# Kernel optimization log

Measured on AMD Instinct MI355X. Metric: run time of the kernel, lower is better.

## Reference

```python
import jax, jax.numpy as jnp
import numpy as np

H = 16          # num_attention_heads
D = 64          # attention_head_size
BUCKET = 128    # bucket_size
MAX_BUCKETS = 32
TEMP = 0.75
SINKHORN_ITERS = 5
NOISE_KEY = 42  # fixed key for gumbel routing noise (deterministic reference)


def _sinkhorn_route(pl, W, key):
    # pl: [b,h,buckets,d] bucket summaries, W: [h,d,buckets]
    R = jnp.einsum('bhid,hdf->bhif', pl, W)  # [b,h,buckets,buckets]
    u = jax.random.uniform(key, R.shape, R.dtype)
    gumbel = -jnp.log(-jnp.log(u + 1e-6) + 1e-6)
    R = (R + gumbel) / TEMP
    for _ in range(SINKHORN_ITERS):
        R = R - jax.scipy.special.logsumexp(R, axis=-1, keepdims=True)
        R = R - jax.scipy.special.logsumexp(R, axis=-2, keepdims=True)
    return jnp.exp(R)


def setup_inputs() -> dict:
    key = jax.random.key(0)
    kq, kk, kv, kwk, kwv = jax.random.split(key, 5)
    q = jax.random.normal(kq, (64, 4096, 64), jnp.float32)
    k = jax.random.normal(kk, (64, 4096, 64), jnp.float32)
    v = jax.random.normal(kv, (64, 4096, 64), jnp.float32)
    W_keys = jax.random.normal(kwk, (H, D, MAX_BUCKETS), jnp.float32)
    W_vals = jax.random.normal(kwv, (H, D, MAX_BUCKETS), jnp.float32)
    return {'q': q, 'k': k, 'v': v, 'W_keys': W_keys, 'W_vals': W_vals}


def reference(q, q_unused=None, *, _=None, **__):
    raise RuntimeError  # placeholder, replaced below


def reference(q, k, v, W_keys, W_vals):
    t, d = q.shape[1], q.shape[2]
    buckets = t // BUCKET
    # [b, h, buckets, bucket_size, d]
    b_q = q.reshape(-1, H, buckets, BUCKET, d)
    b_k = k.reshape(-1, H, buckets, BUCKET, d)
    b_v = v.reshape(-1, H, buckets, BUCKET, d)

    pl_k = b_k.sum(axis=-2)  # [b,h,buckets,d]
    R_k = _sinkhorn_route(pl_k, W_keys[..., :buckets], jax.random.key(NOISE_KEY))
    # NOTE: original also computes R_v / b_v_r but never uses them for output.

    b_k = jnp.einsum('bhij,bhjsd->bhisd', R_k, b_k) + b_k

    dots = jnp.einsum('bhuid,bhujd->bhuij', b_q, b_k) * (d ** -0.5)
    probs = jax.nn.softmax(dots, axis=-1)
    out = jnp.einsum('bhuij,bhujd->bhuid', probs, b_v)  # [b,h,buckets,s,d]
    return out.reshape(-1, t, d)
```

## Files before the change

kernel.cpp:

```cpp
#include <hip/hip_runtime.h>
#include <math.h>

#define BH 64
#define NB 32
#define BS 128
#define DHEAD 64

typedef __attribute__((ext_vector_type(8))) short bf16x8;
typedef __attribute__((ext_vector_type(4))) float f32x4;

#define LDK 72
#define LDVT 128
#define LDP 136

__device__ __forceinline__ unsigned rotl32(unsigned x, int d) {
    return (x << d) | (x >> (32 - d));
}

__device__ __forceinline__ void threefry2x32(unsigned k0, unsigned k1,
                                             unsigned& x0, unsigned& x1) {
    const unsigned ks0 = k0, ks1 = k1, ks2 = k0 ^ k1 ^ 0x1BD11BDAu;
    const int r0[4] = {13, 15, 26, 6};
    const int r1[4] = {17, 29, 16, 24};
    x0 += ks0; x1 += ks1;
    #pragma unroll
    for (int i = 0; i < 4; i++) { x0 += x1; x1 = rotl32(x1, r0[i]); x1 ^= x0; }
    x0 += ks1; x1 += ks2 + 1u;
    #pragma unroll
    for (int i = 0; i < 4; i++) { x0 += x1; x1 = rotl32(x1, r1[i]); x1 ^= x0; }
    x0 += ks2; x1 += ks0 + 2u;
    #pragma unroll
    for (int i = 0; i < 4; i++) { x0 += x1; x1 = rotl32(x1, r0[i]); x1 ^= x0; }
    x0 += ks0; x1 += ks1 + 3u;
    #pragma unroll
    for (int i = 0; i < 4; i++) { x0 += x1; x1 = rotl32(x1, r1[i]); x1 ^= x0; }
    x0 += ks1; x1 += ks2 + 4u;
    #pragma unroll
    for (int i = 0; i < 4; i++) { x0 += x1; x1 = rotl32(x1, r0[i]); x1 ^= x0; }
    x0 += ks2; x1 += ks0 + 5u;
}

__device__ __forceinline__ float jax_uniform_part(unsigned f) {
    unsigned x0 = 0u, x1 = f;
    threefry2x32(0u, 42u, x0, x1);
    unsigned bits = x0 ^ x1;
    return __uint_as_float((bits >> 9) | 0x3F800000u) - 1.0f;
}

__global__ void __launch_bounds__(256)
pl_kernel(const float* __restrict__ k, float* __restrict__ pl) {
    int blk = blockIdx.x;
    int g = threadIdx.x >> 6;
    int d = threadIdx.x & 63;
    const float* kp = k + (size_t)blk * 8192 + (size_t)g * 2048 + d;
    float s = 0.f;
    #pragma unroll
    for (int i = 0; i < 32; i++) s += kp[i * 64];
    __shared__ float red[4][64];
    red[g][d] = s;
    __syncthreads();
    if (threadIdx.x < 64)
        pl[blk * 64 + threadIdx.x] = (red[0][threadIdx.x] + red[1][threadIdx.x])
                                   + (red[2][threadIdx.x] + red[3][threadIdx.x]);
}

__global__ void route_kernel(const float* __restrict__ pl, const float* __restrict__ Wk,
                             float* __restrict__ Rout) {
    int bh = blockIdx.x;
    int h = bh & 15;
    int tid = threadIdx.x;
    int i = tid >> 5, j = tid & 31;

    __shared__ float plS[NB * DHEAD];
    __shared__ float T[32 * 33];
    __shared__ float colL[32];

    for (int x = tid; x < NB * DHEAD; x += 1024) plS[x] = pl[bh * NB * DHEAD + x];
    __syncthreads();

    float acc = 0.f;
    #pragma unroll 8
    for (int d2 = 0; d2 < DHEAD; d2++)
        acc += plS[i * DHEAD + d2] * Wk[(h * DHEAD + d2) * NB + j];

    unsigned f = (unsigned)bh * 1024u + (unsigned)i * 32u + (unsigned)j;
    float u = jax_uniform_part(f);
    float g = -logf(-logf(u + 1e-6f) + 1e-6f);
    float val = (acc + g) / 0.75f;

    for (int it = 0; it < 5; it++) {
        float m = val;
        #pragma unroll
        for (int off = 1; off < 32; off <<= 1) m = fmaxf(m, __shfl_xor(m, off, 32));
        float s = expf(val - m);
        #pragma unroll
        for (int off = 1; off < 32; off <<= 1) s += __shfl_xor(s, off, 32);
        val -= m + logf(s);

        T[i * 33 + j] = val;
        __syncthreads();
        float tv = T[j * 33 + i];
        float m2 = tv;
        #pragma unroll
        for (int off = 1; off < 32; off <<= 1) m2 = fmaxf(m2, __shfl_xor(m2, off, 32));
        float s2 = expf(tv - m2);
        #pragma unroll
        for (int off = 1; off < 32; off <<= 1) s2 += __shfl_xor(s2, off, 32);
        if (j == 0) colL[i] = m2 + logf(s2);
        __syncthreads();
        val -= colL[j];
    }
    Rout[bh * 1024 + i * 32 + j] = expf(val) + (i == j ? 1.0f : 0.0f);
}

__global__ void __launch_bounds__(256)
mix_kernel(const float* __restrict__ k, const float* __restrict__ Rp,
           float* __restrict__ Kp) {
    __shared__ float X[32][260];
    int bh = blockIdx.x >> 5;
    int tile = blockIdx.x & 31;
    const size_t kbase = (size_t)bh * 262144;
    const int col0 = tile * 256;

    {
        int j = threadIdx.x >> 3;
        int cs = (threadIdx.x & 7) * 32;
        const float4* src = (const float4*)(k + kbase + (size_t)j * 8192 + col0 + cs);
        #pragma unroll
        for (int t = 0; t < 8; t++)
            *((float4*)&X[j][cs + 4 * t]) = src[t];
    }
    __syncthreads();

    const int col = threadIdx.x;
    float xv[32];
    #pragma unroll
    for (int j = 0; j < 32; j++) xv[j] = X[j][col];

    const float* Rb = Rp + bh * 1024;
    float* outp = Kp + kbase + col0 + col;
    #pragma unroll 4
    for (int i = 0; i < 32; i++) {
        float acc = 0.f;
        #pragma unroll
        for (int j = 0; j < 32; j++) acc = fmaf(Rb[i * 32 + j], xv[j], acc);
        outp[(size_t)i * 8192] = acc;
    }
}

__global__ void __launch_bounds__(256)
attn_mfma_kernel(const float* __restrict__ q, const float* __restrict__ Kp,
                 const float* __restrict__ v, float* __restrict__ out) {
    __shared__ __align__(16) unsigned short smem[2 * 128 * LDK + 64 * LDVT];
    unsigned short* KhS = smem;
    unsigned short* KlS = smem + 128 * LDK;
    unsigned short* VtS = smem + 256 * LDK;
    unsigned short* PbS = smem;

    const int tid = threadIdx.x;
    const int w = tid >> 6, lane = tid & 63;
    const int quad = lane >> 4, l15 = lane & 15;
    const int row0 = 32 * w;
    const size_t base = (size_t)blockIdx.x * (BS * DHEAD);

    bf16x8 qh[2][2], ql[2][2];
    #pragma unroll
    for (int ti = 0; ti < 2; ti++) {
        #pragma unroll
        for (int kk = 0; kk < 2; kk++) {
            const float* qp = q + base + (size_t)(row0 + 16 * ti + l15) * DHEAD
                              + kk * 32 + quad * 8;
            float4 a = ((const float4*)qp)[0];
            float4 b = ((const float4*)qp)[1];
            float f[8] = {a.x, a.y, a.z, a.w, b.x, b.y, b.z, b.w};
            #pragma unroll
            for (int j = 0; j < 8; j++) {
                float qs = f[j] * 0.125f;
                unsigned bits = __float_as_uint(qs);
                unsigned short hi = (unsigned short)(bits >> 16);
                float rem = qs - __uint_as_float(bits & 0xFFFF0000u);
                unsigned short lo = (unsigned short)(__float_as_uint(rem) >> 16);
                qh[ti][kk][j] = (short)hi;
                ql[ti][kk][j] = (short)lo;
            }
        }
    }

    {
        int r = tid >> 1, c0 = (tid & 1) * 32;
        const float* kp = Kp + base + (size_t)r * DHEAD + c0;
        #pragma unroll
        for (int x = 0; x < 8; x++) {
            float4 a = ((const float4*)kp)[x];
            float kf[4] = {a.x, a.y, a.z, a.w};
            #pragma unroll
            for (int y = 0; y < 4; y++) {
                int c = c0 + 4 * x + y;
                unsigned kb = __float_as_uint(kf[y]);
                unsigned short hi = (unsigned short)(kb >> 16);
                float rem = kf[y] - __uint_as_float(kb & 0xFFFF0000u);
                unsigned short lo = (unsigned short)(__float_as_uint(rem) >> 16);
                KhS[r * LDK + c] = hi;
                KlS[r * LDK + c] = lo;
            }
        }
    }

    {
        int rp = tid >> 2;
        int c0 = (tid & 3) * 16;
        const float* v0 = v + base + (size_t)(2 * rp) * DHEAD + c0;
        const float* v1 = v0 + DHEAD;
        #pragma unroll
        for (int x = 0; x < 4; x++) {
            float4 a = ((const float4*)v0)[x];
            float4 b = ((const float4*)v1)[x];
            float fa[4] = {a.x, a.y, a.z, a.w};
            float fb[4] = {b.x, b.y, b.z, b.w};
            #pragma unroll
            for (int y = 0; y < 4; y++) {
                int c = c0 + 4 * x + y;
                unsigned lo = (__float_as_uint(fa[y]) + 0x8000u) >> 16;
                unsigned hi = (__float_as_uint(fb[y]) + 0x8000u) >> 16;
                unsigned swz = ((unsigned)((c ^ (c >> 4)) & 15)) << 3;
                unsigned idx = (unsigned)c * LDVT + (((unsigned)(2 * rp)) ^ swz);
                *(unsigned*)&VtS[idx] = lo | (hi << 16);
            }
        }
    }
    __syncthreads();

    f32x4 acc[2][8];
    #pragma unroll
    for (int ti = 0; ti < 2; ti++)
        #pragma unroll
        for (int tc = 0; tc < 8; tc++)
            acc[ti][tc] = (f32x4){0.f, 0.f, 0.f, 0.f};

    #pragma unroll
    for (int tc = 0; tc < 8; tc++) {
        const int jrow = 16 * tc + l15;
        bf16x8 bh0 = *(const bf16x8*)&KhS[jrow * LDK + 0  + quad * 8];
        bf16x8 bh1 = *(const bf16x8*)&KhS[jrow * LDK + 32 + quad * 8];
        bf16x8 bl0 = *(const bf16x8*)&KlS[jrow * LDK + 0  + quad * 8];
        bf16x8 bl1 = *(const bf16x8*)&KlS[jrow * LDK + 32 + quad * 8];
        #pragma unroll
        for (int ti = 0; ti < 2; ti++) {
            f32x4 c = acc[ti][tc];
            c = __builtin_amdgcn_mfma_f32_16x16x32_bf16(qh[ti][0], bh0, c, 0, 0, 0);
            c = __builtin_amdgcn_mfma_f32_16x16x32_bf16(qh[ti][1], bh1, c, 0, 0, 0);
            c = __builtin_amdgcn_mfma_f32_16x16x32_bf16(ql[ti][0], bh0, c, 0, 0, 0);
            c = __builtin_amdgcn_mfma_f32_16x16x32_bf16(ql[ti][1], bh1, c, 0, 0, 0);
            c = __builtin_amdgcn_mfma_f32_16x16x32_bf16(qh[ti][0], bl0, c, 0, 0, 0);
            c = __builtin_amdgcn_mfma_f32_16x16x32_bf16(qh[ti][1], bl1, c, 0, 0, 0);
            acc[ti][tc] = c;
        }
    }

    float mrow[2][4], lrow[2][4];
    #pragma unroll
    for (int ti = 0; ti < 2; ti++)
        #pragma unroll
        for (int r = 0; r < 4; r++) {
            float m = acc[ti][0][r];
            #pragma unroll
            for (int tc = 1; tc < 8; tc++) m = fmaxf(m, acc[ti][tc][r]);
            #pragma unroll
            for (int off = 1; off < 16; off <<= 1)
                m = fmaxf(m, __shfl_xor(m, off, 64));
            mrow[ti][r] = m;
        }
    #pragma unroll
    for (int ti = 0; ti < 2; ti++)
        #pragma unroll
        for (int r = 0; r < 4; r++) {
            float s = 0.f;
            #pragma unroll
            for (int tc = 0; tc < 8; tc++) {
                float p = __expf(acc[ti][tc][r] - mrow[ti][r]);
                acc[ti][tc][r] = p;
                s += p;
            }
            #pragma unroll
            for (int off = 1; off < 16; off <<= 1)
                s += __shfl_xor(s, off, 64);
            lrow[ti][r] = s;
        }

    __syncthreads();

    #pragma unroll
    for (int ti = 0; ti < 2; ti++)
        #pragma unroll
        for (int tc = 0; tc < 8; tc++)
            #pragma unroll
            for (int r = 0; r < 4; r++) {
                int prow = row0 + 16 * ti + quad * 4 + r;
                unsigned pb = __float_as_uint(acc[ti][tc][r]);
                PbS[prow * LDP + 16 * tc + l15] = (unsigned short)((pb + 0x8000u) >> 16);
            }
    __syncthreads();

    f32x4 oacc[2][4];
    #pragma unroll
    for (int ti = 0; ti < 2; ti++)
        #pragma unroll
        for (int tc = 0; tc < 4; tc++)
            oacc[ti][tc] = (f32x4){0.f, 0.f, 0.f, 0.f};

    #pragma unroll
    for (int kc = 0; kc < 4; kc++) {
        bf16x8 aP[2];
        #pragma unroll
        for (int ti = 0; ti < 2; ti++)
            aP[ti] = *(const bf16x8*)&PbS[(row0 + 16 * ti + l15) * LDP + kc * 32 + quad * 8];
        #pragma unroll
        for (int tc = 0; tc < 4; tc++) {
            unsigned n = (unsigned)(16 * tc + l15);
            unsigned swz = ((n ^ (n >> 4)) & 15u) << 3;
            unsigned idx = n * LDVT + (((unsigned)(kc * 32 + quad * 8)) ^ swz);
            bf16x8 vb = *(const bf16x8*)&VtS[idx];
            #pragma unroll
            for (int ti = 0; ti < 2; ti++)
                oacc[ti][tc] = __builtin_amdgcn_mfma_f32_16x16x32_bf16(aP[ti], vb, oacc[ti][tc], 0, 0, 0);
        }
    }

    float inv[2][4];
    #pragma unroll
    for (int ti = 0; ti < 2; ti++)
        #pragma unroll
        for (int r = 0; r < 4; r++) inv[ti][r] = 1.0f / lrow[ti][r];

    #pragma unroll
    for (int ti = 0; ti < 2; ti++)
        #pragma unroll
        for (int tc = 0; tc < 4; tc++)
            #pragma unroll
            for (int r = 0; r < 4; r++) {
                int orow = row0 + 16 * ti + quad * 4 + r;
                out[base + (size_t)orow * DHEAD + 16 * tc + l15] = oacc[ti][tc][r] * inv[ti][r];
            }
}

extern "C" void kernel_launch(void* const* d_in, const int* in_sizes, int n_in,
                              void* d_out, int out_size, void* d_ws, size_t ws_size,
                              hipStream_t stream) {
    const float* q  = (const float*)d_in[0];
    const float* k  = (const float*)d_in[1];
    const float* v  = (const float*)d_in[2];
    const float* Wk = (const float*)d_in[3];
    float* out = (float*)d_out;

    float* Kp = (float*)d_ws;
    float* pl = Kp + (size_t)16777216;
    float* R  = pl + (size_t)131072;

    pl_kernel<<<dim3(BH * NB), dim3(256), 0, stream>>>(k, pl);
    route_kernel<<<dim3(BH), dim3(1024), 0, stream>>>(pl, Wk, R);
    mix_kernel<<<dim3(BH * NB), dim3(256), 0, stream>>>(k, R, Kp);
    attn_mfma_kernel<<<dim3(BH * NB), dim3(256), 0, stream>>>(q, Kp, v, out);
}
```

Baseline: 294.6 us.

## Emit pre-split swizzled bf16 hi/lo keys from mix kernel and DMA into LDS

```diff
diff --git a/kernel.cpp b/kernel.cpp
--- a/kernel.cpp
+++ b/kernel.cpp
@@ -9,9 +9,9 @@
 typedef __attribute__((ext_vector_type(8))) short bf16x8;
 typedef __attribute__((ext_vector_type(4))) float f32x4;
 
-#define LDK 72
 #define LDVT 128
 #define LDP 136
+
 
 __device__ __forceinline__ unsigned rotl32(unsigned x, int d) {
     return (x << d) | (x >> (32 - d));
@@ -115,7 +115,7 @@
 
 __global__ void __launch_bounds__(256)
 mix_kernel(const float* __restrict__ k, const float* __restrict__ Rp,
-           float* __restrict__ Kp) {
+           unsigned short* __restrict__ khl) {
     __shared__ float X[32][260];
     int bh = blockIdx.x >> 5;
     int tile = blockIdx.x & 31;
@@ -138,30 +138,73 @@
     for (int j = 0; j < 32; j++) xv[j] = X[j][col];
 
     const float* Rb = Rp + bh * 1024;
-    float* outp = Kp + kbase + col0 + col;
+    const int slot = col0 + col;
+    const int s = slot >> 6, d = slot & 63;
+    const int idx = s * 64 + (d ^ ((s & 7) << 3));
+
     #pragma unroll 4
     for (int i = 0; i < 32; i++) {
         float acc = 0.f;
         #pragma unroll
         for (int j = 0; j < 32; j++) acc = fmaf(Rb[i * 32 + j], xv[j], acc);
-        outp[(size_t)i * 8192] = acc;
+        unsigned kb = __float_as_uint(acc);
+        unsigned short hi = (unsigned short)(kb >> 16);
+        float rem = acc - __uint_as_float(kb & 0xFFFF0000u);
+        unsigned short lo = (unsigned short)(__float_as_uint(rem) >> 16);
+        unsigned short* bp = khl + ((size_t)(bh * 32 + i) << 14);
+        bp[idx] = hi;
+        bp[idx + 8192] = lo;
     }
 }
 
 __global__ void __launch_bounds__(256)
-attn_mfma_kernel(const float* __restrict__ q, const float* __restrict__ Kp,
+attn_mfma_kernel(const float* __restrict__ q, const unsigned short* __restrict__ khl,
                  const float* __restrict__ v, float* __restrict__ out) {
-    __shared__ __align__(16) unsigned short smem[2 * 128 * LDK + 64 * LDVT];
-    unsigned short* KhS = smem;
-    unsigned short* KlS = smem + 128 * LDK;
-    unsigned short* VtS = smem + 256 * LDK;
-    unsigned short* PbS = smem;
+    __shared__ __align__(16) unsigned short smem[8192 + 17408];
+    unsigned short* VtS = smem;
+    unsigned short* KhS = smem + 8192;
+    unsigned short* KlS = smem + 16384;
+    unsigned short* PbS = smem + 8192;
 
     const int tid = threadIdx.x;
     const int w = tid >> 6, lane = tid & 63;
     const int quad = lane >> 4, l15 = lane & 15;
     const int row0 = 32 * w;
     const size_t base = (size_t)blockIdx.x * (BS * DHEAD);
+
+    {
+        const char* src = (const char*)(khl + ((size_t)blockIdx.x << 14)) + tid * 16;
+        char* dst = (char*)KhS + tid * 16;
+        #pragma unroll
+        for (int c = 0; c < 8; c++)
+            __builtin_amdgcn_global_load_lds(
+                (const __attribute__((address_space(1))) unsigned int*)(src + c * 4096),
+                (__attribute__((address_space(3))) unsigned int*)(dst + c * 4096),
+                16, 0, 0);
+    }
+
+    {
+        int rp = tid >> 2;
+        int c0 = (tid & 3) * 16;
+        const float* v0 = v + base + (size_t)(2 * rp) * DHEAD + c0;
+        const float* v1 = v0 + DHEAD;
+        #pragma unroll
+        for (int x = 0; x < 4; x++) {
+            float4 a = ((const float4*)v0)[x];
+            float4 b = ((const float4*)v1)[x];
+            float fa[4] = {a.x, a.y, a.z, a.w};
+            float fb[4] = {b.x, b.y, b.z, b.w};
+            #pragma unroll
+            for (int y = 0; y < 4; y++) {
+                int c = c0 + 4 * x + y;
+                unsigned lo = (__float_as_uint(fa[y]) + 0x8000u) >> 16;
+                unsigned hi = (__float_as_uint(fb[y]) + 0x8000u) >> 16;
+                unsigned swz = ((unsigned)((c ^ (c >> 4)) & 15)) << 3;
+                unsigned idx = (unsigned)c * LDVT + (((unsigned)(2 * rp)) ^ swz);
+                *(unsigned*)&VtS[idx] = lo | (hi << 16);
+            }
+        }
+    }
 
     bf16x8 qh[2][2], ql[2][2];
     #pragma unroll
@@ -185,49 +228,6 @@
             }
         }
     }
-
-    {
-        int r = tid >> 1, c0 = (tid & 1) * 32;
-        const float* kp = Kp + base + (size_t)r * DHEAD + c0;
-        #pragma unroll
-        for (int x = 0; x < 8; x++) {
-            float4 a = ((const float4*)kp)[x];
-            float kf[4] = {a.x, a.y, a.z, a.w};
-            #pragma unroll
-            for (int y = 0; y < 4; y++) {
-                int c = c0 + 4 * x + y;
-                unsigned kb = __float_as_uint(kf[y]);
-                unsigned short hi = (unsigned short)(kb >> 16);
-                float rem = kf[y] - __uint_as_float(kb & 0xFFFF0000u);
-                unsigned short lo = (unsigned short)(__float_as_uint(rem) >> 16);
-                KhS[r * LDK + c] = hi;
-                KlS[r * LDK + c] = lo;
-            }
-        }
-    }
-
-    {
-        int rp = tid >> 2;
-        int c0 = (tid & 3) * 16;
-        const float* v0 = v + base + (size_t)(2 * rp) * DHEAD + c0;
-        const float* v1 = v0 + DHEAD;
-        #pragma unroll
-        for (int x = 0; x < 4; x++) {
-            float4 a = ((const float4*)v0)[x];
-            float4 b = ((const float4*)v1)[x];
-            float fa[4] = {a.x, a.y, a.z, a.w};
-            float fb[4] = {b.x, b.y, b.z, b.w};
-            #pragma unroll
-            for (int y = 0; y < 4; y++) {
-                int c = c0 + 4 * x + y;
-                unsigned lo = (__float_as_uint(fa[y]) + 0x8000u) >> 16;
-                unsigned hi = (__float_as_uint(fb[y]) + 0x8000u) >> 16;
-                unsigned swz = ((unsigned)((c ^ (c >> 4)) & 15)) << 3;
-                unsigned idx = (unsigned)c * LDVT + (((unsigned)(2 * rp)) ^ swz);
-                *(unsigned*)&VtS[idx] = lo | (hi << 16);
-            }
-        }
-    }
     __syncthreads();
 
     f32x4 acc[2][8];
@@ -240,10 +240,13 @@
     #pragma unroll
     for (int tc = 0; tc < 8; tc++) {
         const int jrow = 16 * tc + l15;
-        bf16x8 bh0 = *(const bf16x8*)&KhS[jrow * LDK + 0  + quad * 8];
-        bf16x8 bh1 = *(const bf16x8*)&KhS[jrow * LDK + 32 + quad * 8];
-        bf16x8 bl0 = *(const bf16x8*)&KlS[jrow * LDK + 0  + quad * 8];
-        bf16x8 bl1 = *(const bf16x8*)&KlS[jrow * LDK + 32 + quad * 8];
+        const int swzk = (jrow & 7) << 3;
+        const int rbase = jrow * 64;
+        bf16x8 bh0 = *(const bf16x8*)&KhS[rbase + ((quad * 8 + 0)  ^ swzk)];
+        bf16x8 bh1 = *(const bf16x8*)&KhS[rbase + ((quad * 8 + 32) ^ swzk)];
+        bf16x8 bl0 = *(const bf16x8*)&KlS[rbase + ((quad * 8 + 0)  ^ swzk)];
+        bf16x8 bl1 = *(const bf16x8*)&KlS[rbase + ((quad * 8 + 32) ^ swzk)];
+        __builtin_amdgcn_s_setprio(1);
         #pragma unroll
         for (int ti = 0; ti < 2; ti++) {
             f32x4 c = acc[ti][tc];
@@ -255,6 +258,7 @@
             c = __builtin_amdgcn_mfma_f32_16x16x32_bf16(qh[ti][1], bl1, c, 0, 0, 0);
             acc[ti][tc] = c;
         }
+        __builtin_amdgcn_s_setprio(0);
     }
 
     float mrow[2][4], lrow[2][4];
@@ -314,6 +318,7 @@
         #pragma unroll
         for (int ti = 0; ti < 2; ti++)
             aP[ti] = *(const bf16x8*)&PbS[(row0 + 16 * ti + l15) * LDP + kc * 32 + quad * 8];
+        __builtin_amdgcn_s_setprio(1);
         #pragma unroll
         for (int tc = 0; tc < 4; tc++) {
             unsigned n = (unsigned)(16 * tc + l15);
@@ -324,6 +329,7 @@
             for (int ti = 0; ti < 2; ti++)
                 oacc[ti][tc] = __builtin_amdgcn_mfma_f32_16x16x32_bf16(aP[ti], vb, oacc[ti][tc], 0, 0, 0);
         }
+        __builtin_amdgcn_s_setprio(0);
     }
 
     float inv[2][4];
@@ -352,12 +358,12 @@
     const float* Wk = (const float*)d_in[3];
     float* out = (float*)d_out;
 
-    float* Kp = (float*)d_ws;
-    float* pl = Kp + (size_t)16777216;
+    unsigned short* khl = (unsigned short*)d_ws;
+    float* pl = (float*)(khl + (size_t)33554432);
     float* R  = pl + (size_t)131072;
 
     pl_kernel<<<dim3(BH * NB), dim3(256), 0, stream>>>(k, pl);
     route_kernel<<<dim3(BH), dim3(1024), 0, stream>>>(pl, Wk, R);
-    mix_kernel<<<dim3(BH * NB), dim3(256), 0, stream>>>(k, R, Kp);
-    attn_mfma_kernel<<<dim3(BH * NB), dim3(256), 0, stream>>>(q, Kp, v, out);
-}
+    mix_kernel<<<dim3(BH * NB), dim3(256), 0, stream>>>(k, R, khl);
+    attn_mfma_kernel<<<dim3(BH * NB), dim3(256), 0, stream>>>(q, khl, v, out);
+}
```

After: 289.6 us. No clear change (-1.7%).
